# Optimization experiments

Measured on AMD Instinct MI355X. Metric: run time of the kernel, lower is better.

The kernel has to match this reference:

```python
import jax, jax.numpy as jnp
import numpy as np

B, C, H, W = 128, 3, 256, 256
SHIFT = int(H * 0.125 + 0.5)   # 32, translation ratio=0.125
CS = int(H * 0.5 + 0.5)        # 128, cutout ratio=0.5 (square images)


def setup_inputs() -> dict:
    key = jax.random.key(0)
    k = jax.random.split(key, 8)
    return {
        "imgs": jax.random.uniform(k[0], (B, C, H, W), dtype=jnp.float32),
        "br": jax.random.uniform(k[1], (B, 1, 1, 1), dtype=jnp.float32),
        "sat": jax.random.uniform(k[2], (B, 1, 1, 1), dtype=jnp.float32),
        "con": jax.random.uniform(k[3], (B, 1, 1, 1), dtype=jnp.float32),
        "tx": jax.random.randint(k[4], (B, 1, 1), 0, 2 * SHIFT + 1, dtype=jnp.int32),
        "ty": jax.random.randint(k[5], (B, 1, 1), 0, 2 * SHIFT + 1, dtype=jnp.int32),
        "cx": jax.random.randint(k[6], (B, 1, 1), 0, H + 1, dtype=jnp.int32),
        "cy": jax.random.randint(k[7], (B, 1, 1), 0, W + 1, dtype=jnp.int32),
    }


def _augment(x, br, sat, con, tx, ty, cx, cy):
    # --- color: brightness, saturation, contrast (same order as AUGMENT_FNS['color']) ---
    x = x + (br - 0.5)
    m = x.mean(axis=1, keepdims=True)                 # channel mean
    x = (x - m) * (sat * 2.0) + m
    m = x.mean(axis=(1, 2, 3), keepdims=True)         # per-image mean
    x = (x - m) * (con + 0.5) + m

    # --- translation (ratio=0.125): pad by 1, clamped gather ---
    txs = tx - SHIFT                                   # in [-SHIFT, SHIFT], [B,1,1]
    tys = ty - SHIFT
    gx = jnp.clip(jnp.arange(H, dtype=jnp.int32)[None, :, None] + txs + 1, 0, H + 1)  # [B,H,1]
    gy = jnp.clip(jnp.arange(W, dtype=jnp.int32)[None, None, :] + tys + 1, 0, W + 1)  # [B,1,W]
    x_pad = jnp.pad(x, ((0, 0), (0, 0), (1, 1), (1, 1)))
    bidx = jnp.arange(B)[:, None, None, None]
    cidx = jnp.arange(C)[None, :, None, None]
    x = x_pad[bidx, cidx, gx[:, None, :, :], gy[:, None, :, :]]  # [B,C,H,W]

    # --- cutout (ratio=0.5): zero a CS x CS clamped window per image ---
    grid_x = jnp.clip(jnp.arange(CS, dtype=jnp.int32)[None, :, None] + cx - CS // 2, 0, H - 1)  # [B,CS,1]
    grid_y = jnp.clip(jnp.arange(CS, dtype=jnp.int32)[None, None, :] + cy - CS // 2, 0, W - 1)  # [B,1,CS]
    mask = jnp.ones((B, H, W), x.dtype).at[jnp.arange(B)[:, None, None], grid_x, grid_y].set(0.0)
    return x * mask[:, None, :, :]


def reference(imgs, br, sat, con, tx, ty, cx, cy):
    return _augment(imgs, br, sat, con, tx, ty, cx, cy)
```

## Files before the change

### kernel.cpp

```cpp
#include <hip/hip_runtime.h>

constexpr int BN  = 128;
constexpr int CN  = 3;
constexpr int HN  = 256;
constexpr int WN  = 256;
constexpr int HW  = HN * WN;
constexpr int CHW = CN * HW;
constexpr int SHIFT_ = 32;
constexpr int CS  = 128;
constexpr int RBLK = 8;

__global__ __launch_bounds__(256) void aug_reduce(const float* __restrict__ x,
                                                  float* __restrict__ partial) {
    const int j = blockIdx.x;
    const int b = blockIdx.y;
    const int t = threadIdx.x;
    constexpr int PER_BLOCK = CHW / 4 / RBLK;
    const float4* p = reinterpret_cast<const float4*>(x + (size_t)b * CHW)
                      + (size_t)j * PER_BLOCK;
    float s = 0.f;
    for (int i = t; i < PER_BLOCK; i += 256) {
        float4 v = p[i];
        s += (v.x + v.y) + (v.z + v.w);
    }
    __shared__ float sm[256];
    sm[t] = s;
    __syncthreads();
    #pragma unroll
    for (int off = 128; off > 0; off >>= 1) {
        if (t < off) sm[t] += sm[t + off];
        __syncthreads();
    }
    if (t == 0) partial[b * RBLK + j] = sm[0];
}

__global__ __launch_bounds__(256) void aug_apply(
    const float* __restrict__ x,
    const float* __restrict__ br, const float* __restrict__ sat,
    const float* __restrict__ con,
    const int* __restrict__ tx, const int* __restrict__ ty,
    const int* __restrict__ cx, const int* __restrict__ cy,
    const float* __restrict__ partial, float* __restrict__ out)
{
    const int b  = blockIdx.y;
    const int g  = blockIdx.x * 256 + threadIdx.x;
    const int p0 = g << 2;
    const int h  = p0 >> 8;
    const int w0 = p0 & (WN - 1);

    __shared__ float s_gm;
    if (threadIdx.x == 0) {
        float s = 0.f;
        #pragma unroll
        for (int i = 0; i < RBLK; ++i) s += partial[b * RBLK + i];
        s_gm = s * (1.0f / (float)CHW);
    }
    __syncthreads();
    const float gm = s_gm;

    const float b1 = br[b] - 0.5f;
    const float k  = (con[b] + 0.5f) * (sat[b] * 2.0f);
    const float c2 = con[b] + 0.5f;

    const int sh  = h  + (tx[b] - SHIFT_);
    const int sw0 = w0 + (ty[b] - SHIFT_);
    const int cx0 = cx[b] - CS / 2;
    const int cy0 = cy[b] - CS / 2;
    const int h0 = max(cx0, 0), h1 = min(cx0 + CS - 1, HN - 1);
    const int wc0 = max(cy0, 0), wc1 = min(cy0 + CS - 1, WN - 1);

    const bool rowok   = (sh >= 0) & (sh < HN);
    const bool cut_row = (h >= h0) & (h <= h1);
    const bool cut_all = cut_row & (w0 >= wc0) & (w0 + 3 <= wc1);

    float x0[4], x1[4], x2[4];
    bool  valid[4];

    if (rowok & !cut_all) {
        const float* base = x + (size_t)b * CHW + sh * WN + sw0;
        if (sw0 >= 0 && sw0 + 3 < WN) {
            float4 a, bb, c;
            __builtin_memcpy(&a,  base,          sizeof(float4));
            __builtin_memcpy(&bb, base + HW,     sizeof(float4));
            __builtin_memcpy(&c,  base + 2 * HW, sizeof(float4));
            x0[0]=a.x;  x0[1]=a.y;  x0[2]=a.z;  x0[3]=a.w;
            x1[0]=bb.x; x1[1]=bb.y; x1[2]=bb.z; x1[3]=bb.w;
            x2[0]=c.x;  x2[1]=c.y;  x2[2]=c.z;  x2[3]=c.w;
            #pragma unroll
            for (int i = 0; i < 4; ++i) valid[i] = true;
        } else {
            #pragma unroll
            for (int i = 0; i < 4; ++i) {
                const int sw = sw0 + i;
                const bool ok = (sw >= 0) & (sw < WN);
                valid[i] = ok;
                if (ok) {
                    x0[i] = base[i];
                    x1[i] = base[i + HW];
                    x2[i] = base[i + 2 * HW];
                } else {
                    x0[i] = x1[i] = x2[i] = 0.f;
                }
            }
        }
    } else {
        #pragma unroll
        for (int i = 0; i < 4; ++i) { x0[i]=x1[i]=x2[i]=0.f; valid[i]=false; }
    }

    float4 o0, o1, o2;
    float* po0 = &o0.x; float* po1 = &o1.x; float* po2 = &o2.x;
    #pragma unroll
    for (int i = 0; i < 4; ++i) {
        const int w = w0 + i;
        const bool cut = cut_row & (w >= wc0) & (w <= wc1);
        const bool live = valid[i] & !cut;
        const float cm  = (x0[i] + x1[i] + x2[i]) * (1.0f / 3.0f);
        const float add = c2 * (cm - gm) + gm + b1;
        po0[i] = live ? (k * (x0[i] - cm) + add) : 0.f;
        po1[i] = live ? (k * (x1[i] - cm) + add) : 0.f;
        po2[i] = live ? (k * (x2[i] - cm) + add) : 0.f;
    }

    float4* ob = reinterpret_cast<float4*>(out + (size_t)b * CHW + p0);
    ob[0]          = o0;
    ob[HW / 4]     = o1;
    ob[2 * HW / 4] = o2;
}

extern "C" void kernel_launch(void* const* d_in, const int* in_sizes, int n_in,
                              void* d_out, int out_size, void* d_ws, size_t ws_size,
                              hipStream_t stream) {
    const float* imgs = (const float*)d_in[0];
    const float* br   = (const float*)d_in[1];
    const float* sat  = (const float*)d_in[2];
    const float* con  = (const float*)d_in[3];
    const int*   tx   = (const int*)d_in[4];
    const int*   ty   = (const int*)d_in[5];
    const int*   cx   = (const int*)d_in[6];
    const int*   cy   = (const int*)d_in[7];
    float* out = (float*)d_out;
    float* partial = (float*)d_ws;

    aug_reduce<<<dim3(RBLK, BN), 256, 0, stream>>>(imgs, partial);
    aug_apply<<<dim3(HW / 4 / 256, BN), 256, 0, stream>>>(imgs, br, sat, con,
                                                          tx, ty, cx, cy, partial, out);
}
```

Measured before the change: 198.5 us.

## Fuse reduce and apply into one cooperative kernel with grid sync

Replaces the two launches (per-image partial sums, then apply) with one cooperative kernel. Each of 1024 blocks first computes its partial sum, a grid-wide sync follows, and the blocks then loop over the apply tiles. Output stores become nontemporal. The aim is to drop the second launch and the gap between kernels. In exchange it adds grid-barrier cost, and the launch requires all 1024 blocks to be co-resident (4 per CU requested via launch bounds).

```diff
diff --git a/kernel.cpp b/kernel.cpp
--- a/kernel.cpp
+++ b/kernel.cpp
@@ -1,4 +1,7 @@
 #include <hip/hip_runtime.h>
+#include <hip/hip_cooperative_groups.h>
+
+namespace cg = cooperative_groups;
 
 constexpr int BN  = 128;
 constexpr int CN  = 3;
@@ -9,123 +12,126 @@
 constexpr int SHIFT_ = 32;
 constexpr int CS  = 128;
 constexpr int RBLK = 8;
+constexpr int GRID = BN * RBLK;
+constexpr int TILES = BN * (HW / 4 / 256);
 
-__global__ __launch_bounds__(256) void aug_reduce(const float* __restrict__ x,
-                                                  float* __restrict__ partial) {
-    const int j = blockIdx.x;
-    const int b = blockIdx.y;
-    const int t = threadIdx.x;
-    constexpr int PER_BLOCK = CHW / 4 / RBLK;
-    const float4* p = reinterpret_cast<const float4*>(x + (size_t)b * CHW)
-                      + (size_t)j * PER_BLOCK;
-    float s = 0.f;
-    for (int i = t; i < PER_BLOCK; i += 256) {
-        float4 v = p[i];
-        s += (v.x + v.y) + (v.z + v.w);
-    }
-    __shared__ float sm[256];
-    sm[t] = s;
-    __syncthreads();
-    #pragma unroll
-    for (int off = 128; off > 0; off >>= 1) {
-        if (t < off) sm[t] += sm[t + off];
-        __syncthreads();
-    }
-    if (t == 0) partial[b * RBLK + j] = sm[0];
-}
+typedef float vfloat4 __attribute__((ext_vector_type(4)));
 
-__global__ __launch_bounds__(256) void aug_apply(
+__global__ __launch_bounds__(256, 4) void aug_fused(
     const float* __restrict__ x,
     const float* __restrict__ br, const float* __restrict__ sat,
     const float* __restrict__ con,
     const int* __restrict__ tx, const int* __restrict__ ty,
     const int* __restrict__ cx, const int* __restrict__ cy,
-    const float* __restrict__ partial, float* __restrict__ out)
+    float* __restrict__ partial, float* __restrict__ out)
 {
-    const int b  = blockIdx.y;
-    const int g  = blockIdx.x * 256 + threadIdx.x;
-    const int p0 = g << 2;
-    const int h  = p0 >> 8;
-    const int w0 = p0 & (WN - 1);
+    const int blk = blockIdx.x;
+    const int t   = threadIdx.x;
 
-    __shared__ float s_gm;
-    if (threadIdx.x == 0) {
+    {
+        const int b = blk >> 3;
+        const int j = blk & 7;
+        constexpr int PER_BLOCK = CHW / 4 / RBLK;
+        const float4* p = reinterpret_cast<const float4*>(x + (size_t)b * CHW)
+                          + (size_t)j * PER_BLOCK;
+        float s = 0.f;
+        for (int i = t; i < PER_BLOCK; i += 256) {
+            float4 v = p[i];
+            s += (v.x + v.y) + (v.z + v.w);
+        }
+        __shared__ float sm[256];
+        sm[t] = s;
+        __syncthreads();
+        #pragma unroll
+        for (int off = 128; off > 0; off >>= 1) {
+            if (t < off) sm[t] += sm[t + off];
+            __syncthreads();
+        }
+        if (t == 0) partial[b * RBLK + j] = sm[0];
+    }
+
+    cg::this_grid().sync();
+
+    for (int tile = blk; tile < TILES; tile += GRID) {
+        const int b  = tile >> 6;
+        const int g  = ((tile & 63) << 8) + t;
+        const int p0 = g << 2;
+        const int h  = p0 >> 8;
+        const int w0 = p0 & (WN - 1);
+
         float s = 0.f;
         #pragma unroll
         for (int i = 0; i < RBLK; ++i) s += partial[b * RBLK + i];
-        s_gm = s * (1.0f / (float)CHW);
-    }
-    __syncthreads();
-    const float gm = s_gm;
+        const float gm = s * (1.0f / (float)CHW);
 
-    const float b1 = br[b] - 0.5f;
-    const float k  = (con[b] + 0.5f) * (sat[b] * 2.0f);
-    const float c2 = con[b] + 0.5f;
+        const float b1 = br[b] - 0.5f;
+        const float c2 = con[b] + 0.5f;
+        const float k  = c2 * (sat[b] * 2.0f);
 
-    const int sh  = h  + (tx[b] - SHIFT_);
-    const int sw0 = w0 + (ty[b] - SHIFT_);
-    const int cx0 = cx[b] - CS / 2;
-    const int cy0 = cy[b] - CS / 2;
-    const int h0 = max(cx0, 0), h1 = min(cx0 + CS - 1, HN - 1);
-    const int wc0 = max(cy0, 0), wc1 = min(cy0 + CS - 1, WN - 1);
+        const int sh  = h  + (tx[b] - SHIFT_);
+        const int sw0 = w0 + (ty[b] - SHIFT_);
+        const int cx0 = cx[b] - CS / 2;
+        const int cy0 = cy[b] - CS / 2;
+        const int h0 = max(cx0, 0), h1 = min(cx0 + CS - 1, HN - 1);
+        const int wc0 = max(cy0, 0), wc1 = min(cy0 + CS - 1, WN - 1);
 
-    const bool rowok   = (sh >= 0) & (sh < HN);
-    const bool cut_row = (h >= h0) & (h <= h1);
-    const bool cut_all = cut_row & (w0 >= wc0) & (w0 + 3 <= wc1);
+        const bool rowok   = (sh >= 0) & (sh < HN);
+        const bool cut_row = (h >= h0) & (h <= h1);
+        const bool cut_all = cut_row & (w0 >= wc0) & (w0 + 3 <= wc1);
 
-    float x0[4], x1[4], x2[4];
-    bool  valid[4];
+        float x0[4], x1[4], x2[4];
+        bool  valid[4];
 
-    if (rowok & !cut_all) {
-        const float* base = x + (size_t)b * CHW + sh * WN + sw0;
-        if (sw0 >= 0 && sw0 + 3 < WN) {
-            float4 a, bb, c;
-            __builtin_memcpy(&a,  base,          sizeof(float4));
-            __builtin_memcpy(&bb, base + HW,     sizeof(float4));
-            __builtin_memcpy(&c,  base + 2 * HW, sizeof(float4));
-            x0[0]=a.x;  x0[1]=a.y;  x0[2]=a.z;  x0[3]=a.w;
-            x1[0]=bb.x; x1[1]=bb.y; x1[2]=bb.z; x1[3]=bb.w;
-            x2[0]=c.x;  x2[1]=c.y;  x2[2]=c.z;  x2[3]=c.w;
-            #pragma unroll
-            for (int i = 0; i < 4; ++i) valid[i] = true;
+        if (rowok & !cut_all) {
+            const float* base = x + (size_t)b * CHW + sh * WN + sw0;
+            if (sw0 >= 0 && sw0 + 3 < WN) {
+                float4 a, bb, c;
+                __builtin_memcpy(&a,  base,          sizeof(float4));
+                __builtin_memcpy(&bb, base + HW,     sizeof(float4));
+                __builtin_memcpy(&c,  base + 2 * HW, sizeof(float4));
+                x0[0]=a.x;  x0[1]=a.y;  x0[2]=a.z;  x0[3]=a.w;
+                x1[0]=bb.x; x1[1]=bb.y; x1[2]=bb.z; x1[3]=bb.w;
+                x2[0]=c.x;  x2[1]=c.y;  x2[2]=c.z;  x2[3]=c.w;
+                #pragma unroll
+                for (int i = 0; i < 4; ++i) valid[i] = true;
+            } else {
+                #pragma unroll
+                for (int i = 0; i < 4; ++i) {
+                    const int sw = sw0 + i;
+                    const bool ok = (sw >= 0) & (sw < WN);
+                    valid[i] = ok;
+                    if (ok) {
+                        x0[i] = base[i];
+                        x1[i] = base[i + HW];
+                        x2[i] = base[i + 2 * HW];
+                    } else {
+                        x0[i] = x1[i] = x2[i] = 0.f;
+                    }
+                }
+            }
         } else {
             #pragma unroll
-            for (int i = 0; i < 4; ++i) {
-                const int sw = sw0 + i;
-                const bool ok = (sw >= 0) & (sw < WN);
-                valid[i] = ok;
-                if (ok) {
-                    x0[i] = base[i];
-                    x1[i] = base[i + HW];
-                    x2[i] = base[i + 2 * HW];
-                } else {
-                    x0[i] = x1[i] = x2[i] = 0.f;
-                }
-            }
+            for (int i = 0; i < 4; ++i) { x0[i]=x1[i]=x2[i]=0.f; valid[i]=false; }
         }
-    } else {
+
+        vfloat4 o0, o1, o2;
         #pragma unroll
-        for (int i = 0; i < 4; ++i) { x0[i]=x1[i]=x2[i]=0.f; valid[i]=false; }
+        for (int i = 0; i < 4; ++i) {
+            const int w = w0 + i;
+            const bool cut = cut_row & (w >= wc0) & (w <= wc1);
+            const bool live = valid[i] & !cut;
+            const float cm  = (x0[i] + x1[i] + x2[i]) * (1.0f / 3.0f);
+            const float add = c2 * (cm - gm) + gm + b1;
+            o0[i] = live ? (k * (x0[i] - cm) + add) : 0.f;
+            o1[i] = live ? (k * (x1[i] - cm) + add) : 0.f;
+            o2[i] = live ? (k * (x2[i] - cm) + add) : 0.f;
+        }
+
+        vfloat4* ob = reinterpret_cast<vfloat4*>(out + (size_t)b * CHW + p0);
+        __builtin_nontemporal_store(o0, ob);
+        __builtin_nontemporal_store(o1, ob + HW / 4);
+        __builtin_nontemporal_store(o2, ob + 2 * HW / 4);
     }
-
-    float4 o0, o1, o2;
-    float* po0 = &o0.x; float* po1 = &o1.x; float* po2 = &o2.x;
-    #pragma unroll
-    for (int i = 0; i < 4; ++i) {
-        const int w = w0 + i;
-        const bool cut = cut_row & (w >= wc0) & (w <= wc1);
-        const bool live = valid[i] & !cut;
-        const float cm  = (x0[i] + x1[i] + x2[i]) * (1.0f / 3.0f);
-        const float add = c2 * (cm - gm) + gm + b1;
-        po0[i] = live ? (k * (x0[i] - cm) + add) : 0.f;
-        po1[i] = live ? (k * (x1[i] - cm) + add) : 0.f;
-        po2[i] = live ? (k * (x2[i] - cm) + add) : 0.f;
-    }
-
-    float4* ob = reinterpret_cast<float4*>(out + (size_t)b * CHW + p0);
-    ob[0]          = o0;
-    ob[HW / 4]     = o1;
-    ob[2 * HW / 4] = o2;
 }
 
 extern "C" void kernel_launch(void* const* d_in, const int* in_sizes, int n_in,
@@ -142,7 +148,9 @@
     float* out = (float*)d_out;
     float* partial = (float*)d_ws;
 
-    aug_reduce<<<dim3(RBLK, BN), 256, 0, stream>>>(imgs, partial);
-    aug_apply<<<dim3(HW / 4 / 256, BN), 256, 0, stream>>>(imgs, br, sat, con,
-                                                          tx, ty, cx, cy, partial, out);
+    void* args[] = { (void*)&imgs, (void*)&br, (void*)&sat, (void*)&con,
+                     (void*)&tx, (void*)&ty, (void*)&cx, (void*)&cy,
+                     (void*)&partial, (void*)&out };
+    (void)hipLaunchCooperativeKernel((void*)aug_fused, dim3(GRID), dim3(256),
+                                     args, 0, stream);
 }
```

Measured after the change: 278.7 us. +40.4%, slower.
